# Optimization experiments

Measured on AMD Instinct MI355X. Metric: run time of the kernel, lower is better.

The kernel has to match this reference:

```python
import jax, jax.numpy as jnp
import numpy as np

B, N, DIM = 16, 1024, 768
H = 12
HD = DIM // H
SCALE = HD ** -0.5

def setup_inputs() -> dict:
    key = jax.random.key(0)
    k1, k2, k3, k4 = jax.random.split(key, 4)
    x = jax.random.normal(k1, (B, N, DIM), dtype=jnp.float32)
    # qkv: Linear(dim, 3*dim, bias=False); torch weight is [out, in]
    w_qkv = jax.random.normal(k2, (3 * DIM, DIM), dtype=jnp.float32) * (DIM ** -0.5)
    # proj: Linear(dim, dim) with bias
    w_proj = jax.random.normal(k3, (DIM, DIM), dtype=jnp.float32) * (DIM ** -0.5)
    b_proj = jax.random.normal(k4, (DIM,), dtype=jnp.float32) * 0.02
    return {"x": x, "w_qkv": w_qkv, "w_proj": w_proj, "b_proj": b_proj}

def reference(x, w_qkv, w_proj, b_proj):
    B_, N_, D_ = x.shape
    # qkv projection: [B, N, 3*D] -> [3, B, H, N, HD]
    qkv = jnp.einsum('bnd,ed->bne', x, w_qkv)
    qkv = qkv.reshape(B_, N_, 3, H, HD).transpose(2, 0, 3, 1, 4)
    q, k, v = qkv[0], qkv[1], qkv[2]
    # attention scores [B, H, N, N]
    attn = jnp.einsum('bhqd,bhkd->bhqk', q, k) * SCALE
    attn = jax.nn.softmax(attn, axis=-1)
    # weighted values -> [B, N, D]
    out = jnp.einsum('bhqk,bhkd->bhqd', attn, v)
    out = out.transpose(0, 2, 1, 3).reshape(B_, N_, D_)
    # output projection
    out = jnp.einsum('bnd,ed->bne', out, w_proj) + b_proj
    return out
```

## Files before the change

kernel.cpp:

```cpp
#include <hip/hip_runtime.h>
#include <cstdint>

#define B_SZ 16
#define SEQ 1024
#define DIM 768
#define NH 12
#define HD 64
#define M_TOTAL (B_SZ*SEQ)
#define QKV_OUT (3*DIM)
#define EXP2_SCALE 0.18033688011f

typedef _Float16 f16;
typedef __attribute__((ext_vector_type(8))) f16 f16x8;
typedef __attribute__((ext_vector_type(4))) f16 f16x4;
typedef __attribute__((ext_vector_type(2))) __fp16 pk16x2;
typedef __attribute__((ext_vector_type(4))) short s4_t;
typedef __attribute__((ext_vector_type(4))) float f32x4;
typedef unsigned int u32;
typedef const __attribute__((address_space(1))) u32* gas_t;
typedef __attribute__((address_space(3))) u32* las_t;

union U4 { pk16x2 h2[2]; f16x4 v; };
union U8 { pk16x2 h2[4]; f16x8 v; };
union HS { f16 h; short s; };

__device__ __forceinline__ void async16(const void* g, void* l) {
    __builtin_amdgcn_global_load_lds((gas_t)g, (las_t)l, 16, 0, 0);
}
__device__ __forceinline__ f32x4 mfma32h(f16x8 a, f16x8 b, f32x4 c) {
    return __builtin_amdgcn_mfma_f32_16x16x32_f16(a, b, c, 0, 0, 0);
}
__device__ __forceinline__ f16x8 ldfragh(const short* p) {
    return *(const f16x8*)p;
}

__global__ void cvt_kernel(const float* __restrict__ x, const float* __restrict__ wq,
                           const float* __restrict__ wp,
                           short* __restrict__ xb, short* __restrict__ wqb, short* __restrict__ wpb) {
    const long nx = (long)M_TOTAL * DIM / 4;
    const long nq = (long)QKV_OUT * DIM / 4;
    const long np = (long)DIM * DIM / 4;
    const long total = nx + nq + np;
    for (long i = (long)blockIdx.x * blockDim.x + threadIdx.x; i < total;
         i += (long)gridDim.x * blockDim.x) {
        const float4* src; short* dst; long off;
        if (i < nx)            { src = (const float4*)x;  dst = xb;  off = i; }
        else if (i < nx + nq)  { src = (const float4*)wq; dst = wqb; off = i - nx; }
        else                   { src = (const float4*)wp; dst = wpb; off = i - nx - nq; }
        float4 v = src[off];
        U4 u;
        u.h2[0] = __builtin_amdgcn_cvt_pkrtz(v.x, v.y);
        u.h2[1] = __builtin_amdgcn_cvt_pkrtz(v.z, v.w);
        *(f16x4*)(dst + off * 4) = u.v;
    }
}

template<int QM, int QN>
__device__ __forceinline__ void mfma_quad(f32x4 (&acc)[8][4], const f16x8 (&af)[4],
                                          const f16x8 (&bf)[4]) {
#pragma unroll
    for (int r = 0; r < 4; ++r)
#pragma unroll
        for (int c = 0; c < 2; ++c)
            acc[QM * 4 + r][QN * 2 + c] = mfma32h(af[r], bf[QN * 2 + c], acc[QM * 4 + r][QN * 2 + c]);
}

template<int EPI, int N, int K>
__global__ __launch_bounds__(512, 2) void gemm_bt(const short* __restrict__ A,
                                                  const short* __restrict__ Bm,
                                                  short* __restrict__ Cq, short* __restrict__ Ck,
                                                  short* __restrict__ Cv,
                                                  float* __restrict__ Cout,
                                                  const float* __restrict__ bias) {
    static_assert(K % 64 == 0, "even K-tile count required");
    constexpr int NT = K / 32;
    constexpr int NIT = NT / 2;
    __shared__ short lds[32768];

    const int tid = threadIdx.x;
    const int l = tid & 63, quad = l >> 4, l15 = l & 15;
    const int w = tid >> 6, wr = w >> 2, wc = w & 3;
    const int fl = (l15 & 3) ^ ((l15 >> 2) & 3);

    const int gx = gridDim.x;
    const int nwg = gx * (int)gridDim.y;
    int fid = (int)blockIdx.y * gx + (int)blockIdx.x;
    fid = (fid & 7) * (nwg >> 3) + (fid >> 3);
    const int m0 = (fid / gx) * 256;
    const int n0 = (fid % gx) * 256;

    const int srow = tid >> 2, sc = tid & 3;
    const int scc = sc ^ ((srow & 3) ^ ((srow >> 2) & 3));
    const short* Asrc = A + (size_t)(m0 + srow) * K + scc * 8;
    const short* Bsrc = Bm + (size_t)(n0 + srow) * K + scc * 8;
    const int sdst = srow * 32 + sc * 8;

#define STAGE_A(t, hi) async16(Asrc + (size_t)((hi) * 128) * K + (t) * 32, \
                               &lds[((t) & 1) * 16384 + (hi) * 4096 + sdst])
#define STAGE_B(t, hi) async16(Bsrc + (size_t)((hi) * 128) * K + (t) * 32, \
                               &lds[((t) & 1) * 16384 + 8192 + (hi) * 4096 + sdst])

    const int aoff = wr * 4096 + l15 * 32;
    const int boff = 8192 + wc * 2048 + l15 * 32;
    const int c0 = (quad ^ fl) * 8;

#define RD_A(SB, MH) do {                                  \
        const int ab_ = (SB) + aoff + (MH) * 2048;         \
        af[0] = ldfragh(&lds[ab_ + c0]);                   \
        af[1] = ldfragh(&lds[ab_ + 512 + c0]);             \
        af[2] = ldfragh(&lds[ab_ + 1024 + c0]);            \
        af[3] = ldfragh(&lds[ab_ + 1536 + c0]);            \
    } while (0)
#define RD_B(SB, NH) do {                                  \
        const int bb_ = (SB) + boff + (NH) * 1024;         \
        bf[(NH) * 2]     = ldfragh(&lds[bb_ + c0]);        \
        bf[(NH) * 2 + 1] = ldfragh(&lds[bb_ + 512 + c0]);  \
    } while (0)

#define BAR1() __builtin_amdgcn_s_barrier()
#define BAR2() do { __builtin_amdgcn_s_barrier(); __builtin_amdgcn_sched_barrier(0); } while (0)
#define VMC2() asm volatile("s_waitcnt vmcnt(2)" ::: "memory")
#define VMC0() asm volatile("s_waitcnt vmcnt(0)" ::: "memory")
#define MQ(QM, QN) do {                                        \
        __builtin_amdgcn_s_setprio(1);                         \
        mfma_quad<QM, QN>(acc, af, bf);                        \
        __builtin_amdgcn_s_setprio(0);                         \
    } while (0)

    f32x4 acc[8][4];
#pragma unroll
    for (int i = 0; i < 8; ++i)
#pragma unroll
        for (int j = 0; j < 4; ++j) acc[i][j] = (f32x4){0.f, 0.f, 0.f, 0.f};
    f16x8 af[4], bf[4];

    STAGE_B(0, 0); STAGE_B(0, 1); STAGE_A(0, 0); STAGE_A(0, 1);
    STAGE_B(1, 0); STAGE_B(1, 1);
    VMC2();
    BAR2();

    for (int i = 0; i < NIT; ++i) {
        const int to = 2 * i + 1, t2 = 2 * i + 2, t3 = 2 * i + 3;
        RD_A(0, 0); RD_B(0, 0);
        STAGE_A(to, 0);
        BAR1(); MQ(0, 0); BAR2();

        RD_B(0, 1);
        STAGE_A(to, 1);
        BAR1(); MQ(0, 1); BAR2();

        RD_A(0, 1);
        if (t2 < NT) STAGE_B(t2, 0);
        BAR1(); MQ(1, 0); BAR2();

        if (t2 < NT) STAGE_B(t2, 1);
        BAR1(); MQ(1, 1);
        if (i == NIT - 1) VMC0(); else VMC2();
        BAR2();

        RD_A(16384, 0); RD_B(16384, 0);
        if (t2 < NT) STAGE_A(t2, 0);
        BAR1(); MQ(0, 0); BAR2();

        RD_B(16384, 1);
        if (t2 < NT) STAGE_A(t2, 1);
        BAR1(); MQ(0, 1); BAR2();

        RD_A(16384, 1);
        if (t3 < NT) STAGE_B(t3, 0);
        BAR1(); MQ(1, 0); BAR2();

        if (t3 < NT) STAGE_B(t3, 1);
        BAR1(); MQ(1, 1);
        if (i == NIT - 1) VMC0(); else VMC2();
        BAR2();
    }
#undef STAGE_A
#undef STAGE_B
#undef RD_A
#undef RD_B

#pragma unroll
    for (int rt = 0; rt < 8; ++rt) {
        const int mrow = m0 + wr * 128 + (rt >> 2) * 64 + (rt & 3) * 16 + quad * 4;
#pragma unroll
        for (int ct = 0; ct < 4; ++ct) {
            const int col = n0 + wc * 64 + (ct >> 1) * 32 + (ct & 1) * 16 + l15;
            if (EPI == 0) {
                int s = col / DIM;
                int h = (col - s * DIM) >> 6, hd = col & 63;
                int b = mrow >> 10, nn = mrow & 1023;
                if (s == 2) {
                    U4 u;
                    u.h2[0] = __builtin_amdgcn_cvt_pkrtz(acc[rt][ct][0], acc[rt][ct][1]);
                    u.h2[1] = __builtin_amdgcn_cvt_pkrtz(acc[rt][ct][2], acc[rt][ct][3]);
                    *(f16x4*)&Cv[(((size_t)b * NH + h) * HD + hd) * SEQ + nn] = u.v;
                } else {
                    short* dst = (s == 0) ? Cq : Ck;
                    const float qs = (s == 0) ? EXP2_SCALE : 1.0f;
#pragma unroll
                    for (int r = 0; r < 4; ++r) {
                        HS t; t.h = (f16)(acc[rt][ct][r] * qs);
                        dst[(((size_t)b * NH + h) * SEQ + nn + r) * HD + hd] = t.s;
                    }
                }
            } else {
                float bv = bias[col];
#pragma unroll
                for (int r = 0; r < 4; ++r)
                    Cout[(size_t)(mrow + r) * N + col] = acc[rt][ct][r] + bv;
            }
        }
    }
}

__global__ __launch_bounds__(256) void attn_kernel(const short* __restrict__ Q,
                                                   const short* __restrict__ Km,
                                                   const short* __restrict__ Vt,
                                                   short* __restrict__ O) {
    __shared__ short lds[4][4096];
    const int tid = threadIdx.x;
    const int w = tid >> 6, l = tid & 63, quad = l >> 4, l15 = l & 15;
    const int bid = blockIdx.x;
    const int xcd = bid & 7, kk = bid >> 3;
    const int head = xcd + 8 * (kk >> 2);
    const int q0 = (kk & 3) * 256 + w * 64;
    const int b = head / NH, h = head - b * NH;
    const short* Qp = Q + (size_t)head * (SEQ * HD);
    const short* Kp = Km + (size_t)head * (SEQ * HD);
    const short* Vp = Vt + (size_t)head * (SEQ * HD);

    f16x8 qf[4][2];
#pragma unroll
    for (int qt = 0; qt < 4; ++qt)
#pragma unroll
        for (int hf = 0; hf < 2; ++hf)
            qf[qt][hf] = *(const f16x8*)&Qp[(q0 + qt * 16 + l15) * HD + hf * 32 + quad * 8];

    f32x4 oacc[4][4];
#pragma unroll
    for (int qt = 0; qt < 4; ++qt)
#pragma unroll
        for (int ht = 0; ht < 4; ++ht) oacc[qt][ht] = (f32x4){0.f, 0.f, 0.f, 0.f};
    float psum[4] = {0.f, 0.f, 0.f, 0.f};

    const int kr = tid >> 3, kc = tid & 7;
    const int kcc = kc ^ ((kr & 3) ^ (((kr >> 3) & 3) << 1));
    const short* kSrc = Kp + kr * HD + kcc * 8;
    const int kDst = kr * 64 + kc * 8;
    const int vr = tid >> 2, vc = tid & 3;
    const int vcc = vc ^ ((vr >> 1) & 3);
    const short* vSrc = Vp + vr * SEQ + vcc * 8;
    const int vDst = 2048 + vr * 32 + vc * 8;

#define STAGE(bf, g) do {                                   \
        async16(kSrc + (g) * (32 * HD), &lds[bf][kDst]);    \
        async16(vSrc + (g) * 32, &lds[bf][vDst]);           \
    } while (0)

    const int rA = 8 * (l15 >> 2) + (l15 & 3);
    const int sk = (l15 & 3) ^ ((l15 >> 2) << 1);
    const int offK = rA * 64 + ((quad ^ sk) * 8);
    const int offV = 2048 + l15 * 32 + ((quad ^ ((l15 >> 1) & 3)) * 8);

    STAGE(0, 0); STAGE(1, 1); STAGE(2, 2);

    for (int g = 0; g < 32; ++g) {
        if (g <= 29)      asm volatile("s_waitcnt vmcnt(4)" ::: "memory");
        else if (g == 30) asm volatile("s_waitcnt vmcnt(2)" ::: "memory");
        else              asm volatile("s_waitcnt vmcnt(0)" ::: "memory");
        __builtin_amdgcn_s_barrier();
        if (g < 29) STAGE((g + 3) & 3, g + 3);

        const short* kb = &lds[g & 3][0];
        f16x8 kA0 = ldfragh(kb + offK);
        f16x8 kA1 = ldfragh(kb + (offK ^ 32));
        f16x8 kB0 = ldfragh(kb + offK + 256);
        f16x8 kB1 = ldfragh(kb + (offK ^ 32) + 256);
        f16x8 v0 = ldfragh(kb + offV);
        f16x8 v1 = ldfragh(kb + offV + 512);
        f16x8 v2 = ldfragh(kb + offV + 1024);
        f16x8 v3 = ldfragh(kb + offV + 1536);

        __builtin_amdgcn_s_setprio(1);
#pragma unroll
        for (int qt = 0; qt < 4; ++qt) {
            f32x4 sA = (f32x4){0.f, 0.f, 0.f, 0.f};
            sA = mfma32h(kA0, qf[qt][0], sA);
            sA = mfma32h(kA1, qf[qt][1], sA);
            f32x4 sB = (f32x4){0.f, 0.f, 0.f, 0.f};
            sB = mfma32h(kB0, qf[qt][0], sB);
            sB = mfma32h(kB1, qf[qt][1], sB);
            float eA0 = __builtin_amdgcn_exp2f(sA[0]);
            float eA1 = __builtin_amdgcn_exp2f(sA[1]);
            float eA2 = __builtin_amdgcn_exp2f(sA[2]);
            float eA3 = __builtin_amdgcn_exp2f(sA[3]);
            float eB0 = __builtin_amdgcn_exp2f(sB[0]);
            float eB1 = __builtin_amdgcn_exp2f(sB[1]);
            float eB2 = __builtin_amdgcn_exp2f(sB[2]);
            float eB3 = __builtin_amdgcn_exp2f(sB[3]);
            psum[qt] += ((eA0 + eA1) + (eA2 + eA3)) + ((eB0 + eB1) + (eB2 + eB3));
            U8 u;
            u.h2[0] = __builtin_amdgcn_cvt_pkrtz(eA0, eA1);
            u.h2[1] = __builtin_amdgcn_cvt_pkrtz(eA2, eA3);
            u.h2[2] = __builtin_amdgcn_cvt_pkrtz(eB0, eB1);
            u.h2[3] = __builtin_amdgcn_cvt_pkrtz(eB2, eB3);
            oacc[qt][0] = mfma32h(v0, u.v, oacc[qt][0]);
            oacc[qt][1] = mfma32h(v1, u.v, oacc[qt][1]);
            oacc[qt][2] = mfma32h(v2, u.v, oacc[qt][2]);
            oacc[qt][3] = mfma32h(v3, u.v, oacc[qt][3]);
        }
        __builtin_amdgcn_s_setprio(0);
    }
#undef STAGE

#pragma unroll
    for (int qt = 0; qt < 4; ++qt) {
        psum[qt] += __shfl_xor(psum[qt], 16);
        psum[qt] += __shfl_xor(psum[qt], 32);
    }

#pragma unroll
    for (int qt = 0; qt < 4; ++qt) {
        float rinv = 1.0f / psum[qt];
        short* orow = &O[((size_t)b * SEQ + q0 + qt * 16 + l15) * DIM + h * HD + quad * 4];
#pragma unroll
        for (int ht = 0; ht < 4; ++ht) {
            U4 u;
            u.h2[0] = __builtin_amdgcn_cvt_pkrtz(oacc[qt][ht][0] * rinv, oacc[qt][ht][1] * rinv);
            u.h2[1] = __builtin_amdgcn_cvt_pkrtz(oacc[qt][ht][2] * rinv, oacc[qt][ht][3] * rinv);
            *(f16x4*)(orow + ht * 16) = u.v;
        }
    }
}

extern "C" void kernel_launch(void* const* d_in, const int* in_sizes, int n_in,
                              void* d_out, int out_size, void* d_ws, size_t ws_size,
                              hipStream_t stream) {
    const float* x      = (const float*)d_in[0];
    const float* w_qkv  = (const float*)d_in[1];
    const float* w_proj = (const float*)d_in[2];
    const float* b_proj = (const float*)d_in[3];
    float* out = (float*)d_out;

    short* p = (short*)d_ws;
    short* Xb  = p; p += (size_t)M_TOTAL * DIM;
    short* Wqb = p; p += (size_t)QKV_OUT * DIM;
    short* Wpb = p; p += (size_t)DIM * DIM;
    short* Qb  = p; p += (size_t)B_SZ * NH * SEQ * HD;
    short* Kb  = p; p += (size_t)B_SZ * NH * SEQ * HD;
    short* Vtb = p; p += (size_t)B_SZ * NH * SEQ * HD;
    short* Ob  = p; p += (size_t)M_TOTAL * DIM;

    cvt_kernel<<<1024, 256, 0, stream>>>(x, w_qkv, w_proj, Xb, Wqb, Wpb);
    gemm_bt<0, QKV_OUT, DIM><<<dim3(QKV_OUT / 256, M_TOTAL / 256), 512, 0, stream>>>(
        Xb, Wqb, Qb, Kb, Vtb, nullptr, nullptr);
    attn_kernel<<<B_SZ * NH * (SEQ / 256), 256, 0, stream>>>(Qb, Kb, Vtb, Ob);
    gemm_bt<1, DIM, DIM><<<dim3(DIM / 256, M_TOTAL / 256), 512, 0, stream>>>(
        Ob, Wpb, nullptr, nullptr, nullptr, out, b_proj);
}
```

Measured before the change: 282.5 us.

## Retile GEMM to 256x192 blocks with 64-wide K tiles and 4x2 waves

```diff
diff --git a/kernel.cpp b/kernel.cpp
--- a/kernel.cpp
+++ b/kernel.cpp
@@ -55,14 +55,18 @@
     }
 }
 
-template<int QM, int QN>
-__device__ __forceinline__ void mfma_quad(f32x4 (&acc)[8][4], const f16x8 (&af)[4],
-                                          const f16x8 (&bf)[4]) {
-#pragma unroll
-    for (int r = 0; r < 4; ++r)
-#pragma unroll
-        for (int c = 0; c < 2; ++c)
-            acc[QM * 4 + r][QN * 2 + c] = mfma32h(af[r], bf[QN * 2 + c], acc[QM * 4 + r][QN * 2 + c]);
+template<int MH, int NHH>
+__device__ __forceinline__ void mfma_quad(f32x4 (&acc)[4][6], const f16x8 (&af)[2][2],
+                                          const f16x8 (&bf)[3][2]) {
+#pragma unroll
+    for (int r = 0; r < 2; ++r)
+#pragma unroll
+        for (int c = 0; c < 3; ++c) {
+            f32x4 t = acc[MH * 2 + r][NHH * 3 + c];
+            t = mfma32h(af[r][0], bf[c][0], t);
+            t = mfma32h(af[r][1], bf[c][1], t);
+            acc[MH * 2 + r][NHH * 3 + c] = t;
+        }
 }
 
 template<int EPI, int N, int K>
@@ -72,108 +76,120 @@
                                                   short* __restrict__ Cv,
                                                   float* __restrict__ Cout,
                                                   const float* __restrict__ bias) {
-    static_assert(K % 64 == 0, "even K-tile count required");
-    constexpr int NT = K / 32;
+    static_assert(K % 128 == 0, "even K-tile count required");
+    constexpr int NT = K / 64;
     constexpr int NIT = NT / 2;
-    __shared__ short lds[32768];
+    constexpr int SLOT = 28672;
+    __shared__ short lds[2 * SLOT];
 
     const int tid = threadIdx.x;
-    const int l = tid & 63, quad = l >> 4, l15 = l & 15;
-    const int w = tid >> 6, wr = w >> 2, wc = w & 3;
-    const int fl = (l15 & 3) ^ ((l15 >> 2) & 3);
+    const int l = tid & 63, quad = l >> 4, l15 = l & 15, l7 = l15 & 7;
+    const int w = tid >> 6, wr = w >> 1, wc = w & 1;
 
     const int gx = gridDim.x;
     const int nwg = gx * (int)gridDim.y;
     int fid = (int)blockIdx.y * gx + (int)blockIdx.x;
     fid = (fid & 7) * (nwg >> 3) + (fid >> 3);
     const int m0 = (fid / gx) * 256;
-    const int n0 = (fid % gx) * 256;
-
-    const int srow = tid >> 2, sc = tid & 3;
-    const int scc = sc ^ ((srow & 3) ^ ((srow >> 2) & 3));
+    const int n0 = (fid % gx) * 192;
+
+    const int srow = tid >> 3, sc = tid & 7;
+    const int scc = sc ^ (srow & 7);
     const short* Asrc = A + (size_t)(m0 + srow) * K + scc * 8;
     const short* Bsrc = Bm + (size_t)(n0 + srow) * K + scc * 8;
-    const int sdst = srow * 32 + sc * 8;
-
-#define STAGE_A(t, hi) async16(Asrc + (size_t)((hi) * 128) * K + (t) * 32, \
-                               &lds[((t) & 1) * 16384 + (hi) * 4096 + sdst])
-#define STAGE_B(t, hi) async16(Bsrc + (size_t)((hi) * 128) * K + (t) * 32, \
-                               &lds[((t) & 1) * 16384 + 8192 + (hi) * 4096 + sdst])
-
-    const int aoff = wr * 4096 + l15 * 32;
-    const int boff = 8192 + wc * 2048 + l15 * 32;
-    const int c0 = (quad ^ fl) * 8;
-
-#define RD_A(SB, MH) do {                                  \
-        const int ab_ = (SB) + aoff + (MH) * 2048;         \
-        af[0] = ldfragh(&lds[ab_ + c0]);                   \
-        af[1] = ldfragh(&lds[ab_ + 512 + c0]);             \
-        af[2] = ldfragh(&lds[ab_ + 1024 + c0]);            \
-        af[3] = ldfragh(&lds[ab_ + 1536 + c0]);            \
+    const int sdst = tid * 8;
+
+#define STAGE_A(t, u) async16(Asrc + (size_t)((u) * 64) * K + (t) * 64, \
+                              &lds[((t) & 1) * SLOT + (u) * 4096 + sdst])
+#define STAGE_B(t, u) async16(Bsrc + (size_t)((u) * 64) * K + (t) * 64, \
+                              &lds[((t) & 1) * SLOT + 16384 + (u) * 4096 + sdst])
+
+    const int awoff = wr * 4096 + l15 * 64;
+    const int bwoff = 16384 + wc * 6144 + l15 * 64;
+    const int c0 = (quad ^ l7) * 8;
+    const int c1 = ((4 + quad) ^ l7) * 8;
+
+#define RD_A(SB, MH) do {                                      \
+        const int ab_ = (SB) + awoff + (MH) * 2048;            \
+        af[0][0] = ldfragh(&lds[ab_ + c0]);                    \
+        af[0][1] = ldfragh(&lds[ab_ + c1]);                    \
+        af[1][0] = ldfragh(&lds[ab_ + 1024 + c0]);             \
+        af[1][1] = ldfragh(&lds[ab_ + 1024 + c1]);             \
     } while (0)
-#define RD_B(SB, NH) do {                                  \
-        const int bb_ = (SB) + boff + (NH) * 1024;         \
-        bf[(NH) * 2]     = ldfragh(&lds[bb_ + c0]);        \
-        bf[(NH) * 2 + 1] = ldfragh(&lds[bb_ + 512 + c0]);  \
+#define RD_B(SB, NHH) do {                                     \
+        const int bb_ = (SB) + bwoff + (NHH) * 3072;           \
+        bf[0][0] = ldfragh(&lds[bb_ + c0]);                    \
+        bf[0][1] = ldfragh(&lds[bb_ + c1]);                    \
+        bf[1][0] = ldfragh(&lds[bb_ + 1024 + c0]);             \
+        bf[1][1] = ldfragh(&lds[bb_ + 1024 + c1]);             \
+        bf[2][0] = ldfragh(&lds[bb_ + 2048 + c0]);             \
+        bf[2][1] = ldfragh(&lds[bb_ + 2048 + c1]);             \
     } while (0)
 
 #define BAR1() __builtin_amdgcn_s_barrier()
 #define BAR2() do { __builtin_amdgcn_s_barrier(); __builtin_amdgcn_sched_barrier(0); } while (0)
-#define VMC2() asm volatile("s_waitcnt vmcnt(2)" ::: "memory")
+#define VMC3() asm volatile("s_waitcnt vmcnt(3)" ::: "memory")
 #define VMC0() asm volatile("s_waitcnt vmcnt(0)" ::: "memory")
-#define MQ(QM, QN) do {                                        \
+#define MQ(MH, NHH) do {                                       \
         __builtin_amdgcn_s_setprio(1);                         \
-        mfma_quad<QM, QN>(acc, af, bf);                        \
+        mfma_quad<MH, NHH>(acc, af, bf);                       \
         __builtin_amdgcn_s_setprio(0);                         \
     } while (0)
 
-    f32x4 acc[8][4];
-#pragma unroll
-    for (int i = 0; i < 8; ++i)
-#pragma unroll
-        for (int j = 0; j < 4; ++j) acc[i][j] = (f32x4){0.f, 0.f, 0.f, 0.f};
-    f16x8 af[4], bf[4];
-
-    STAGE_B(0, 0); STAGE_B(0, 1); STAGE_A(0, 0); STAGE_A(0, 1);
-    STAGE_B(1, 0); STAGE_B(1, 1);
-    VMC2();
+    f32x4 acc[4][6];
+#pragma unroll
+    for (int i = 0; i < 4; ++i)
+#pragma unroll
+        for (int j = 0; j < 6; ++j) acc[i][j] = (f32x4){0.f, 0.f, 0.f, 0.f};
+    f16x8 af[2][2], bf[3][2];
+
+    STAGE_B(0, 0); STAGE_B(0, 1); STAGE_B(0, 2);
+    STAGE_A(0, 0); STAGE_A(0, 1); STAGE_A(0, 2); STAGE_A(0, 3);
+    STAGE_B(1, 0); STAGE_B(1, 1); STAGE_B(1, 2);
+    VMC3();
     BAR2();
 
+#pragma unroll 1
     for (int i = 0; i < NIT; ++i) {
-        const int to = 2 * i + 1, t2 = 2 * i + 2, t3 = 2 * i + 3;
-        RD_A(0, 0); RD_B(0, 0);
-        STAGE_A(to, 0);
-        BAR1(); MQ(0, 0); BAR2();
-
-        RD_B(0, 1);
-        STAGE_A(to, 1);
-        BAR1(); MQ(0, 1); BAR2();
-
-        RD_A(0, 1);
-        if (t2 < NT) STAGE_B(t2, 0);
-        BAR1(); MQ(1, 0); BAR2();
-
-        if (t2 < NT) STAGE_B(t2, 1);
-        BAR1(); MQ(1, 1);
-        if (i == NIT - 1) VMC0(); else VMC2();
-        BAR2();
-
-        RD_A(16384, 0); RD_B(16384, 0);
-        if (t2 < NT) STAGE_A(t2, 0);
-        BAR1(); MQ(0, 0); BAR2();
-
-        RD_B(16384, 1);
-        if (t2 < NT) STAGE_A(t2, 1);
-        BAR1(); MQ(0, 1); BAR2();
-
-        RD_A(16384, 1);
-        if (t3 < NT) STAGE_B(t3, 0);
-        BAR1(); MQ(1, 0); BAR2();
-
-        if (t3 < NT) STAGE_B(t3, 1);
-        BAR1(); MQ(1, 1);
-        if (i == NIT - 1) VMC0(); else VMC2();
-        BAR2();
+        const int ta = 2 * i, tb = 2 * i + 1;
+        {
+            const int t1 = ta + 1, t2 = ta + 2;
+            RD_A(0, 0); RD_B(0, 0);
+            if (t1 < NT) { STAGE_A(t1, 0); STAGE_A(t1, 1); }
+            BAR1(); MQ(0, 0); BAR2();
+
+            RD_A(0, 1);
+            if (t1 < NT) { STAGE_A(t1, 2); STAGE_A(t1, 3); }
+            BAR1(); MQ(1, 0); BAR2();
+
+            RD_B(0, 1);
+            BAR1(); MQ(1, 1); BAR2();
+
+            RD_A(0, 0);
+            if (t2 < NT) { STAGE_B(t2, 0); STAGE_B(t2, 1); STAGE_B(t2, 2); }
+            BAR1(); MQ(0, 1);
+            if (t2 < NT) VMC3(); else VMC0();
+            BAR2();
+        }
+        {
+            const int t1 = tb + 1, t2 = tb + 2;
+            RD_A(SLOT, 0); RD_B(SLOT, 0);
+            if (t1 < NT) { STAGE_A(t1, 0); STAGE_A(t1, 1); }
+            BAR1(); MQ(0, 0); BAR2();
+
+            RD_A(SLOT, 1);
+            if (t1 < NT) { STAGE_A(t1, 2); STAGE_A(t1, 3); }
+            BAR1(); MQ(1, 0); BAR2();
+
+            RD_B(SLOT, 1);
+            BAR1(); MQ(1, 1); BAR2();
+
+            RD_A(SLOT, 0);
+            if (t2 < NT) { STAGE_B(t2, 0); STAGE_B(t2, 1); STAGE_B(t2, 2); }
+            BAR1(); MQ(0, 1);
+            if (t2 < NT) VMC3(); else VMC0();
+            BAR2();
+        }
     }
 #undef STAGE_A
 #undef STAGE_B
@@ -181,11 +197,11 @@
 #undef RD_B
 
 #pragma unroll
-    for (int rt = 0; rt < 8; ++rt) {
-        const int mrow = m0 + wr * 128 + (rt >> 2) * 64 + (rt & 3) * 16 + quad * 4;
-#pragma unroll
-        for (int ct = 0; ct < 4; ++ct) {
-            const int col = n0 + wc * 64 + (ct >> 1) * 32 + (ct & 1) * 16 + l15;
+    for (int rt = 0; rt < 4; ++rt) {
+        const int mrow = m0 + wr * 64 + (rt >> 1) * 32 + (rt & 1) * 16 + quad * 4;
+#pragma unroll
+        for (int ct = 0; ct < 6; ++ct) {
+            const int col = n0 + wc * 96 + (ct / 3) * 48 + (ct % 3) * 16 + l15;
             if (EPI == 0) {
                 int s = col / DIM;
                 int h = (col - s * DIM) >> 6, hd = col & 63;
@@ -353,9 +369,9 @@
     short* Ob  = p; p += (size_t)M_TOTAL * DIM;
 
     cvt_kernel<<<1024, 256, 0, stream>>>(x, w_qkv, w_proj, Xb, Wqb, Wpb);
-    gemm_bt<0, QKV_OUT, DIM><<<dim3(QKV_OUT / 256, M_TOTAL / 256), 512, 0, stream>>>(
+    gemm_bt<0, QKV_OUT, DIM><<<dim3(QKV_OUT / 192, M_TOTAL / 256), 512, 0, stream>>>(
         Xb, Wqb, Qb, Kb, Vtb, nullptr, nullptr);
     attn_kernel<<<B_SZ * NH * (SEQ / 256), 256, 0, stream>>>(Qb, Kb, Vtb, Ob);
-    gemm_bt<1, DIM, DIM><<<dim3(DIM / 256, M_TOTAL / 256), 512, 0, stream>>>(
+    gemm_bt<1, DIM, DIM><<<dim3(DIM / 192, M_TOTAL / 256), 512, 0, stream>>>(
         Ob, Wpb, nullptr, nullptr, nullptr, out, b_proj);
 }
```

Measured after the change: 275.4 us. 1.03x faster.
